# Kernel tuning notes

Measured on AMD Instinct MI355X. Metric: run time of the kernel, lower is better.

The kernel has to match this reference:

```python
import jax, jax.numpy as jnp
import numpy as np

DIM = 384
NUM_HEADS = 12
HEAD_DIM = 32
MID = NUM_HEADS * HEAD_DIM
RES = (32, 32)


def _relative_position_index(res):
    Hh, Ww = res
    coords = np.stack(np.meshgrid(np.arange(Hh), np.arange(Ww), indexing='ij'))  # 2,H,W
    cf = coords.reshape(2, -1)
    rel = cf[:, :, None] - cf[:, None, :]  # 2,N,N
    rel = rel.transpose(1, 2, 0).astype(np.int64)
    rel[:, :, 0] += Hh - 1
    rel[:, :, 1] += Ww - 1
    rel[:, :, 0] *= 2 * Ww - 1
    return rel.sum(-1)  # N,N


def setup_inputs() -> dict:
    key = jax.random.key(0)
    ks = jax.random.split(key, 8)
    B = 8
    Hh, Ww = RES
    table_size = (2 * Hh - 1) * (2 * Ww - 1)
    x = jax.random.normal(ks[0], (B, DIM, Hh, Ww), dtype=jnp.float32)
    wq = jax.random.normal(ks[1], (MID, DIM), dtype=jnp.float32) * 0.02
    bq = jnp.zeros((MID,), dtype=jnp.float32)
    wkv = jax.random.normal(ks[2], (2 * MID, DIM), dtype=jnp.float32) * 0.02
    bkv = jnp.zeros((2 * MID,), dtype=jnp.float32)
    wproj = jax.random.normal(ks[3], (DIM, MID), dtype=jnp.float32) * 0.02
    bproj = jnp.zeros((DIM,), dtype=jnp.float32)
    bias_table = jax.random.normal(ks[4], (table_size, NUM_HEADS), dtype=jnp.float32) * 0.02
    rel_index = jnp.asarray(_relative_position_index(RES), dtype=jnp.int32)  # N,N
    return {"x": x, "wq": wq, "bq": bq, "wkv": wkv, "bkv": bkv,
            "wproj": wproj, "bproj": bproj, "bias_table": bias_table,
            "rel_index": rel_index}


def reference(x, wq, bq, wkv, bkv, wproj, bproj, bias_table, rel_index):
    B, C, Hh, Ww = x.shape
    N = Hh * Ww
    scale = HEAD_DIM ** -0.5
    xf = x.reshape(B, C, N)  # B,C,N
    # 1x1 convs == channelwise linear
    q = jnp.einsum('oc,bcn->bon', wq, xf) + bq[None, :, None]          # B,MID,N
    kv = jnp.einsum('oc,bcn->bon', wkv, xf) + bkv[None, :, None]       # B,2*MID,N
    q = q.reshape(B, NUM_HEADS, HEAD_DIM, N).transpose(0, 1, 3, 2)     # B,h,N,d
    kv = kv.reshape(B, 2, NUM_HEADS, HEAD_DIM, N)
    k = kv[:, 0].transpose(0, 1, 3, 2)                                  # B,h,N,d
    v = kv[:, 1].transpose(0, 1, 3, 2)                                  # B,h,N,d
    attn = jnp.einsum('bhnd,bhmd->bhnm', q, k) * scale                  # B,h,N,N
    rel_bias = bias_table[rel_index.reshape(-1)].reshape(N, N, NUM_HEADS)
    attn = attn + rel_bias.transpose(2, 0, 1)[None]                     # + h,N,N bias
    attn = jax.nn.softmax(attn, axis=-1)
    out = jnp.einsum('bhnm,bhmd->bhnd', attn, v)                        # B,h,N,d
    out = out.transpose(0, 1, 3, 2).reshape(B, MID, N)                  # B,MID,N
    out = jnp.einsum('om,bmn->bon', wproj, out) + bproj[None, :, None]  # B,DIM,N
    return out.reshape(B, C, Hh, Ww)
```

## Files before the change

kernel.cpp:

```cpp
#include <hip/hip_runtime.h>

typedef __bf16 bf16;
typedef __bf16 bf16x8 __attribute__((ext_vector_type(8)));
typedef __bf16 bf16x4 __attribute__((ext_vector_type(4)));
typedef float  f32x4  __attribute__((ext_vector_type(4)));

static constexpr int NB = 8;
static constexpr int NH = 12;
static constexpr int HD = 32;
static constexpr int NN = 1024;
static constexpr int NC = 384;
static constexpr int NTBL = 3969;

static constexpr float LOG2E = 1.4426950408889634f;
static constexpr float QSC   = (float)(0.17677669529663687 * 1.4426950408889634);

static constexpr size_t XT_N   = (size_t)NB*NN*NC;
static constexpr size_t WQKV_N = (size_t)3*NC*NC;
static constexpr size_t WP_N   = (size_t)NC*NC;
static constexpr size_t QKV_N  = (size_t)NB*NH*NN*HD;

static constexpr size_t XT_OFF   = 0;
static constexpr size_t WQKV_OFF = XT_OFF + XT_N;
static constexpr size_t WP_OFF   = WQKV_OFF + WQKV_N;
static constexpr size_t Q_OFF    = WP_OFF + WP_N;
static constexpr size_t K_OFF    = Q_OFF + QKV_N;
static constexpr size_t V_OFF    = K_OFF + QKV_N;
static constexpr size_t AO_OFF   = V_OFF + QKV_N;

#define MFMA16(a,b,c) __builtin_amdgcn_mfma_f32_16x16x32_bf16(a,b,c,0,0,0)

static __device__ inline float fast_exp2(float x) {
#if __has_builtin(__builtin_amdgcn_exp2f)
    return __builtin_amdgcn_exp2f(x);
#else
    return exp2f(x);
#endif
}

__global__ __launch_bounds__(256) void cast_all_kernel(const float* __restrict__ x,
                                                       const float* __restrict__ wq,
                                                       const float* __restrict__ wkv,
                                                       const float* __restrict__ wproj,
                                                       bf16* __restrict__ xt,
                                                       bf16* __restrict__ wqkv,
                                                       bf16* __restrict__ wp)
{
    __shared__ bf16 T[64][68];
    const int t = threadIdx.x;
    if (blockIdx.x >= 768) {
        const size_t i = ((size_t)(blockIdx.x - 768) * 256 + t) * 4;
        if (i >= WQKV_N + WP_N) return;
        const float* src; bf16* dst;
        if (i < (size_t)NC*NC)      { src = wq + i;                     dst = wqkv + i; }
        else if (i < WQKV_N)        { src = wkv + (i - (size_t)NC*NC);  dst = wqkv + i; }
        else                        { src = wproj + (i - WQKV_N);       dst = wp + (i - WQKV_N); }
        float4 v = *(const float4*)src;
        bf16x4 o; o[0] = (bf16)v.x; o[1] = (bf16)v.y; o[2] = (bf16)v.z; o[3] = (bf16)v.w;
        *(bf16x4*)dst = o;
        return;
    }
    const int bid = blockIdx.x;
    const int b = bid / 96, rem = bid % 96, ct = rem >> 4, nt = rem & 15;
    const int c0 = ct * 64, n0 = nt * 64;
    const float* Xb = x + (size_t)b * NC * NN;
    const int nl = t & 63, c4 = (t >> 6) * 4;
#pragma unroll
    for (int i = 0; i < 4; ++i) {
        const int c = c4 + i * 16;
        bf16x4 v;
#pragma unroll
        for (int j = 0; j < 4; ++j)
            v[j] = (bf16)Xb[(size_t)(c0 + c + j) * NN + n0 + nl];
        *(bf16x4*)&T[nl][c] = v;
    }
    __syncthreads();
    const int n = t >> 2;
#pragma unroll
    for (int i = 0; i < 2; ++i) {
        const int cg = (t & 3) * 8 + i * 32;
        bf16x4 a = *(const bf16x4*)&T[n][cg];
        bf16x4 bv = *(const bf16x4*)&T[n][cg + 4];
        bf16x8 vv = __builtin_shufflevector(a, bv, 0, 1, 2, 3, 4, 5, 6, 7);
        *(bf16x8*)&xt[((size_t)b * NN + n0 + n) * NC + c0 + cg] = vv;
    }
}

__global__ __launch_bounds__(256) void qkv_gemm_kernel(
    const bf16* __restrict__ W, const bf16* __restrict__ Xt,
    const float* __restrict__ bq, const float* __restrict__ bkv,
    bf16* __restrict__ Qd, bf16* __restrict__ Kd, bf16* __restrict__ Vd)
{
    __shared__ bf16 As[64][40];
    __shared__ bf16 Bs[128][40];
    const int t = threadIdx.x;
    const int w = t >> 6, lane = t & 63, g = lane >> 4, l16 = lane & 15;
    const int wm = w >> 1, wn = w & 1;
    const int n0g = blockIdx.x * 128;
    const int b = n0g >> 10, n0 = n0g & 1023;
    const int o0 = blockIdx.y * 64;
    const bf16* Xb = Xt + (size_t)b * NN * NC;

    const int ar = t >> 2, ac = (t & 3) * 8;

    f32x4 acc[2][4] = {};

    bf16x8 aw = *(const bf16x8*)&W[(size_t)(o0 + ar) * NC + ac];
    bf16x8 bw[2];
#pragma unroll
    for (int i = 0; i < 2; ++i) {
        const int s = t + i * 256, r = s >> 2, cc = (s & 3) * 8;
        bw[i] = *(const bf16x8*)&Xb[(size_t)(n0 + r) * NC + cc];
    }

    for (int k0 = 0; k0 < NC; k0 += 32) {
        __syncthreads();
        *(bf16x8*)&As[ar][ac] = aw;
#pragma unroll
        for (int i = 0; i < 2; ++i) {
            const int s = t + i * 256, r = s >> 2, cc = (s & 3) * 8;
            *(bf16x8*)&Bs[r][cc] = bw[i];
        }
        __syncthreads();
        if (k0 + 32 < NC) {
            aw = *(const bf16x8*)&W[(size_t)(o0 + ar) * NC + k0 + 32 + ac];
#pragma unroll
            for (int i = 0; i < 2; ++i) {
                const int s = t + i * 256, r = s >> 2, cc = (s & 3) * 8;
                bw[i] = *(const bf16x8*)&Xb[(size_t)(n0 + r) * NC + k0 + 32 + cc];
            }
        }
        bf16x8 a0 = *(const bf16x8*)&As[wm*32      + l16][g*8];
        bf16x8 a1 = *(const bf16x8*)&As[wm*32 + 16 + l16][g*8];
#pragma unroll
        for (int sn = 0; sn < 4; ++sn) {
            bf16x8 bf = *(const bf16x8*)&Bs[wn*64 + sn*16 + l16][g*8];
            acc[0][sn] = MFMA16(a0, bf, acc[0][sn]);
            acc[1][sn] = MFMA16(a1, bf, acc[1][sn]);
        }
    }

#pragma unroll
    for (int sm = 0; sm < 2; ++sm)
#pragma unroll
    for (int sn = 0; sn < 4; ++sn) {
        const int col   = n0 + wn*64 + sn*16 + l16;
        const int obase = o0 + wm*32 + sm*16 + g*4;
        f32x4 v = acc[sm][sn];
        if (obase < 384) {
            const int hh = obase >> 5, d = obase & 31;
            bf16x4 o4;
#pragma unroll
            for (int r = 0; r < 4; ++r) o4[r] = (bf16)((v[r] + bq[obase + r]) * QSC);
            *(bf16x4*)&Qd[(((size_t)b*NH + hh)*NN + col)*HD + d] = o4;
        } else if (obase < 768) {
            const int oo = obase - 384; const int hh = oo >> 5, d = oo & 31;
            bf16x4 o4;
#pragma unroll
            for (int r = 0; r < 4; ++r) o4[r] = (bf16)(v[r] + bkv[oo + r]);
            *(bf16x4*)&Kd[(((size_t)b*NH + hh)*NN + col)*HD + d] = o4;
        } else {
            const int oo = obase - 768; const int hh = oo >> 5, d = oo & 31;
#pragma unroll
            for (int r = 0; r < 4; ++r)
                Vd[(((size_t)b*NH + hh)*HD + d + r)*NN + col] = (bf16)(v[r] + bkv[obase - 384 + r]);
        }
    }
}

__global__ __launch_bounds__(512, 8) void attn_kernel(
    const bf16* __restrict__ Qg, const bf16* __restrict__ Kg, const bf16* __restrict__ Vg,
    const float* __restrict__ bias_table, bf16* __restrict__ AOt)
{
    __shared__ unsigned int pairTu[63][63];
    __shared__ bf16 Ks[128][40];
    __shared__ bf16 Vs[2][32][72];

    const int t = threadIdx.x;
    const int w = t >> 6, lane = t & 63, g = lane >> 4, l16 = lane & 15;

    const int bid = blockIdx.x;
    const int nid = (bid & 7) * 96 + (bid >> 3);
    const int qt = nid & 7;
    const int hb = nid >> 3;
    const int h = hb % 12, b = hb / 12;

    const bf16* Qb = Qg + ((size_t)(b*NH + h)) * NN * HD;
    const bf16* Kb = Kg + ((size_t)(b*NH + h)) * NN * HD;
    const bf16* Vb = Vg + ((size_t)(b*NH + h)) * HD * NN;

    const int kr = t >> 2, kc2 = (t & 3) * 8;
    const int vd = t >> 4, vmi = (t & 15) * 8;
    const int vsub = vmi >> 6, vmm = vmi & 63;
    const int vqa = ((vmm >> 5) & 1) * 32 + ((vmm >> 2) & 3) * 8 + ((vmm >> 4) & 1) * 4;

    bf16x8 sregK = *(const bf16x8*)&Kb[(size_t)kr * HD + kc2];
    bf16x8 sregV = *(const bf16x8*)&Vb[(size_t)vd * NN + vmi];

    const int q0 = qt * 128;
    const int n_s = q0 + w*16 + l16;
    const bf16x8 qfrag = *(const bf16x8*)&Qb[(size_t)n_s * HD + g*8];

    for (int idx = t; idx < 63 * 62; idx += 512) {
        const int dj = idx / 62, dip = idx % 62;
        bf16 lo = (bf16)(bias_table[(size_t)((dip + 1) * 63 + dj) * NH + h] * LOG2E);
        bf16 hi = (bf16)(bias_table[(size_t)(dip * 63 + dj) * NH + h] * LOG2E);
        pairTu[dj][dip] = (unsigned)__builtin_bit_cast(unsigned short, lo)
                        | ((unsigned)__builtin_bit_cast(unsigned short, hi) << 16);
    }

    const int i1w = (q0 >> 5) + (w >> 1);
    const int j1 = ((w & 1) << 4) | l16;
    const int jA63 = (j1 + 31 - 4*g) * 63;

    bf16x8 vones;
#pragma unroll
    for (int e = 0; e < 8; ++e) vones[e] = (bf16)1.0f;

    f32x4 oacc[2] = {};
    f32x4 oacc_l = {};

    for (int ph = 0; ph < 8; ++ph) {
        __syncthreads();
        *(bf16x8*)&Ks[kr][kc2] = sregK;
        { bf16x4 vlo = __builtin_shufflevector(sregV, sregV, 0, 1, 2, 3);
          bf16x4 vhi = __builtin_shufflevector(sregV, sregV, 4, 5, 6, 7);
          *(bf16x4*)&Vs[vsub][vd][vqa]     = vlo;
          *(bf16x4*)&Vs[vsub][vd][vqa + 8] = vhi; }
        __syncthreads();
        if (ph < 7) {
            const int m1 = (ph + 1) * 128;
            sregK = *(const bf16x8*)&Kb[(size_t)(m1 + kr) * HD + kc2];
            sregV = *(const bf16x8*)&Vb[(size_t)vd * NN + m1 + vmi];
        }

#pragma unroll
        for (int sub = 0; sub < 2; ++sub) {
            const int it = 2 * ph + sub;
            const bf16 (*Vsp)[72] = Vs[sub];
            const int dip = i1w - 2*it + 30;
            const unsigned* pAp = &pairTu[0][0] + jA63 + dip;

            f32x4 bacc[4];
#pragma unroll
            for (int r = 0; r < 4; ++r) {
                const unsigned prA = pAp[-63 * r];
                const unsigned prB = pAp[-63 * r - 1008];
                bacc[0][r] = __uint_as_float(prA << 16);
                bacc[2][r] = __uint_as_float(prA & 0xFFFF0000u);
                bacc[1][r] = __uint_as_float(prB << 16);
                bacc[3][r] = __uint_as_float(prB & 0xFFFF0000u);
            }

            float p[4][4];
#pragma unroll
            for (int sc = 0; sc < 4; ++sc) {
                bf16x8 kf = *(const bf16x8*)&Ks[sub*64 + sc*16 + l16][g*8];
                f32x4 z = MFMA16(kf, qfrag, bacc[sc]);
#pragma unroll
                for (int r = 0; r < 4; ++r) p[sc][r] = fast_exp2(z[r]);
            }

#pragma unroll
            for (int kc = 0; kc < 2; ++kc) {
                bf16x8 pa;
#pragma unroll
                for (int r = 0; r < 4; ++r) {
                    pa[r]     = (bf16)p[2*kc][r];
                    pa[4 + r] = (bf16)p[2*kc + 1][r];
                }
#pragma unroll
                for (int ds = 0; ds < 2; ++ds) {
                    bf16x8 vf = *(const bf16x8*)&Vsp[ds*16 + l16][kc*32 + 8*g];
                    oacc[ds] = MFMA16(pa, vf, oacc[ds]);
                }
                oacc_l = MFMA16(pa, vones, oacc_l);
            }
        }
    }

    float rin[4];
#pragma unroll
    for (int r = 0; r < 4; ++r) rin[r] = 1.0f / oacc_l[r];

    const int nrow = q0 + w*16 + g*4;
#pragma unroll
    for (int ds = 0; ds < 2; ++ds) {
        const int c = h*HD + ds*16 + l16;
#pragma unroll
        for (int r = 0; r < 4; ++r)
            AOt[((size_t)b*NN + nrow + r) * NC + c] = (bf16)(oacc[ds][r] * rin[r]);
    }
}

__global__ __launch_bounds__(256) void proj_gemm_kernel(
    const bf16* __restrict__ W, const bf16* __restrict__ AOt,
    const float* __restrict__ bproj, float* __restrict__ out)
{
    __shared__ bf16 As[64][40];
    __shared__ bf16 Bs[128][40];
    const int t = threadIdx.x;
    const int w = t >> 6, lane = t & 63, g = lane >> 4, l16 = lane & 15;
    const int wm = w >> 1, wn = w & 1;
    const int n0g = blockIdx.x * 128;
    const int b = n0g >> 10, n0 = n0g & 1023;
    const int o0 = blockIdx.y * 64;
    const bf16* Ab = AOt + (size_t)b * NN * NC;

    const int ar = t >> 2, ac = (t & 3) * 8;

    f32x4 acc[2][4] = {};

    bf16x8 aw = *(const bf16x8*)&W[(size_t)(o0 + ar) * NC + ac];
    bf16x8 bw[2];
#pragma unroll
    for (int i = 0; i < 2; ++i) {
        const int s = t + i * 256, r = s >> 2, cc = (s & 3) * 8;
        bw[i] = *(const bf16x8*)&Ab[(size_t)(n0 + r) * NC + cc];
    }

    for (int k0 = 0; k0 < NC; k0 += 32) {
        __syncthreads();
        *(bf16x8*)&As[ar][ac] = aw;
#pragma unroll
        for (int i = 0; i < 2; ++i) {
            const int s = t + i * 256, r = s >> 2, cc = (s & 3) * 8;
            *(bf16x8*)&Bs[r][cc] = bw[i];
        }
        __syncthreads();
        if (k0 + 32 < NC) {
            aw = *(const bf16x8*)&W[(size_t)(o0 + ar) * NC + k0 + 32 + ac];
#pragma unroll
            for (int i = 0; i < 2; ++i) {
                const int s = t + i * 256, r = s >> 2, cc = (s & 3) * 8;
                bw[i] = *(const bf16x8*)&Ab[(size_t)(n0 + r) * NC + k0 + 32 + cc];
            }
        }
        bf16x8 a0 = *(const bf16x8*)&As[wm*32      + l16][g*8];
        bf16x8 a1 = *(const bf16x8*)&As[wm*32 + 16 + l16][g*8];
#pragma unroll
        for (int sn = 0; sn < 4; ++sn) {
            bf16x8 bf = *(const bf16x8*)&Bs[wn*64 + sn*16 + l16][g*8];
            acc[0][sn] = MFMA16(a0, bf, acc[0][sn]);
            acc[1][sn] = MFMA16(a1, bf, acc[1][sn]);
        }
    }

#pragma unroll
    for (int sm = 0; sm < 2; ++sm)
#pragma unroll
    for (int sn = 0; sn < 4; ++sn) {
        const int col   = n0 + wn*64 + sn*16 + l16;
        const int obase = o0 + wm*32 + sm*16 + g*4;
        f32x4 v = acc[sm][sn];
#pragma unroll
        for (int r = 0; r < 4; ++r)
            out[((size_t)b*NC + obase + r)*NN + col] = v[r] + bproj[obase + r];
    }
}

extern "C" void kernel_launch(void* const* d_in, const int* in_sizes, int n_in,
                              void* d_out, int out_size, void* d_ws, size_t ws_size,
                              hipStream_t stream)
{
    const float* x          = (const float*)d_in[0];
    const float* wq         = (const float*)d_in[1];
    const float* bq         = (const float*)d_in[2];
    const float* wkv        = (const float*)d_in[3];
    const float* bkv        = (const float*)d_in[4];
    const float* wproj      = (const float*)d_in[5];
    const float* bproj      = (const float*)d_in[6];
    const float* bias_table = (const float*)d_in[7];
    float* out = (float*)d_out;

    bf16* wsb  = (bf16*)d_ws;
    bf16* Xt   = wsb + XT_OFF;
    bf16* Wqkv = wsb + WQKV_OFF;
    bf16* Wp   = wsb + WP_OFF;
    bf16* Qd   = wsb + Q_OFF;
    bf16* Kd   = wsb + K_OFF;
    bf16* Vd   = wsb + V_OFF;
    bf16* AOt  = wsb + AO_OFF;

    cast_all_kernel<<<dim3(768 + 576), 256, 0, stream>>>(x, wq, wkv, wproj, Xt, Wqkv, Wp);
    qkv_gemm_kernel<<<dim3(64, 18), 256, 0, stream>>>(Wqkv, Xt, bq, bkv, Qd, Kd, Vd);
    attn_kernel<<<dim3(768), 512, 0, stream>>>(Qd, Kd, Vd, bias_table, AOt);
    proj_gemm_kernel<<<dim3(64, 6), 256, 0, stream>>>(Wp, AOt, bproj, out);
}
```

Baseline: 67.40 us.

## Use direct global-to-LDS loads with swizzle and 128x128 tiles in GEMMs

```diff
diff --git a/kernel.cpp b/kernel.cpp
--- a/kernel.cpp
+++ b/kernel.cpp
@@ -36,6 +36,12 @@
 #else
     return exp2f(x);
 #endif
+}
+
+static __device__ __forceinline__ void gload16(const bf16* g, bf16* l) {
+    __builtin_amdgcn_global_load_lds(
+        (const __attribute__((address_space(1))) void*)g,
+        (__attribute__((address_space(3))) void*)l, 16, 0, 0);
 }
 
 __global__ __launch_bounds__(256) void cast_all_kernel(const float* __restrict__ x,
@@ -91,61 +97,50 @@
     const float* __restrict__ bq, const float* __restrict__ bkv,
     bf16* __restrict__ Qd, bf16* __restrict__ Kd, bf16* __restrict__ Vd)
 {
-    __shared__ bf16 As[64][40];
-    __shared__ bf16 Bs[128][40];
+    __shared__ bf16 As[128 * 32];
+    __shared__ bf16 Bs[128 * 32];
     const int t = threadIdx.x;
     const int w = t >> 6, lane = t & 63, g = lane >> 4, l16 = lane & 15;
     const int wm = w >> 1, wn = w & 1;
     const int n0g = blockIdx.x * 128;
     const int b = n0g >> 10, n0 = n0g & 1023;
-    const int o0 = blockIdx.y * 64;
+    const int o0 = blockIdx.y * 128;
     const bf16* Xb = Xt + (size_t)b * NN * NC;
 
-    const int ar = t >> 2, ac = (t & 3) * 8;
-
-    f32x4 acc[2][4] = {};
-
-    bf16x8 aw = *(const bf16x8*)&W[(size_t)(o0 + ar) * NC + ac];
-    bf16x8 bw[2];
-#pragma unroll
-    for (int i = 0; i < 2; ++i) {
-        const int s = t + i * 256, r = s >> 2, cc = (s & 3) * 8;
-        bw[i] = *(const bf16x8*)&Xb[(size_t)(n0 + r) * NC + cc];
-    }
+    const int srow = lane >> 2;
+    const int scol = (((lane & 3) ^ ((lane >> 3) & 3))) * 8;
+    const int rsel = (g ^ ((l16 >> 1) & 3)) * 8;
+
+    f32x4 acc[4][4] = {};
 
     for (int k0 = 0; k0 < NC; k0 += 32) {
-        __syncthreads();
-        *(bf16x8*)&As[ar][ac] = aw;
-#pragma unroll
-        for (int i = 0; i < 2; ++i) {
-            const int s = t + i * 256, r = s >> 2, cc = (s & 3) * 8;
-            *(bf16x8*)&Bs[r][cc] = bw[i];
-        }
-        __syncthreads();
-        if (k0 + 32 < NC) {
-            aw = *(const bf16x8*)&W[(size_t)(o0 + ar) * NC + k0 + 32 + ac];
-#pragma unroll
-            for (int i = 0; i < 2; ++i) {
-                const int s = t + i * 256, r = s >> 2, cc = (s & 3) * 8;
-                bw[i] = *(const bf16x8*)&Xb[(size_t)(n0 + r) * NC + k0 + 32 + cc];
-            }
-        }
-        bf16x8 a0 = *(const bf16x8*)&As[wm*32      + l16][g*8];
-        bf16x8 a1 = *(const bf16x8*)&As[wm*32 + 16 + l16][g*8];
-#pragma unroll
-        for (int sn = 0; sn < 4; ++sn) {
-            bf16x8 bf = *(const bf16x8*)&Bs[wn*64 + sn*16 + l16][g*8];
-            acc[0][sn] = MFMA16(a0, bf, acc[0][sn]);
-            acc[1][sn] = MFMA16(a1, bf, acc[1][sn]);
-        }
-    }
-
-#pragma unroll
-    for (int sm = 0; sm < 2; ++sm)
+#pragma unroll
+        for (int j = 0; j < 2; ++j) {
+            const int ra = 32 * w + 16 * j;
+            gload16(&W [(size_t)(o0 + ra + srow) * NC + k0 + scol], &As[ra * 32]);
+            gload16(&Xb[(size_t)(n0 + ra + srow) * NC + k0 + scol], &Bs[ra * 32]);
+        }
+        __syncthreads();
+        bf16x8 a[4], bb[4];
+#pragma unroll
+        for (int s = 0; s < 4; ++s) {
+            a[s]  = *(const bf16x8*)&As[(wm*64 + s*16 + l16) * 32 + rsel];
+            bb[s] = *(const bf16x8*)&Bs[(wn*64 + s*16 + l16) * 32 + rsel];
+        }
+#pragma unroll
+        for (int sm = 0; sm < 4; ++sm)
+#pragma unroll
+            for (int sn = 0; sn < 4; ++sn)
+                acc[sm][sn] = MFMA16(a[sm], bb[sn], acc[sm][sn]);
+        __syncthreads();
+    }
+
+#pragma unroll
+    for (int sm = 0; sm < 4; ++sm)
 #pragma unroll
     for (int sn = 0; sn < 4; ++sn) {
         const int col   = n0 + wn*64 + sn*16 + l16;
-        const int obase = o0 + wm*32 + sm*16 + g*4;
+        const int obase = o0 + wm*64 + sm*16 + g*4;
         f32x4 v = acc[sm][sn];
         if (obase < 384) {
             const int hh = obase >> 5, d = obase & 31;
@@ -252,6 +247,7 @@
                 bacc[3][r] = __uint_as_float(prB & 0xFFFF0000u);
             }
 
+            __builtin_amdgcn_s_setprio(1);
             float p[4][4];
 #pragma unroll
             for (int sc = 0; sc < 4; ++sc) {
@@ -276,6 +272,7 @@
                 }
                 oacc_l = MFMA16(pa, vones, oacc_l);
             }
+            __builtin_amdgcn_s_setprio(0);
         }
     }
 
@@ -297,61 +294,50 @@
     const bf16* __restrict__ W, const bf16* __restrict__ AOt,
     const float* __restrict__ bproj, float* __restrict__ out)
 {
-    __shared__ bf16 As[64][40];
-    __shared__ bf16 Bs[128][40];
+    __shared__ bf16 As[128 * 32];
+    __shared__ bf16 Bs[128 * 32];
     const int t = threadIdx.x;
     const int w = t >> 6, lane = t & 63, g = lane >> 4, l16 = lane & 15;
     const int wm = w >> 1, wn = w & 1;
     const int n0g = blockIdx.x * 128;
     const int b = n0g >> 10, n0 = n0g & 1023;
-    const int o0 = blockIdx.y * 64;
+    const int o0 = blockIdx.y * 128;
     const bf16* Ab = AOt + (size_t)b * NN * NC;
 
-    const int ar = t >> 2, ac = (t & 3) * 8;
-
-    f32x4 acc[2][4] = {};
-
-    bf16x8 aw = *(const bf16x8*)&W[(size_t)(o0 + ar) * NC + ac];
-    bf16x8 bw[2];
-#pragma unroll
-    for (int i = 0; i < 2; ++i) {
-        const int s = t + i * 256, r = s >> 2, cc = (s & 3) * 8;
-        bw[i] = *(const bf16x8*)&Ab[(size_t)(n0 + r) * NC + cc];
-    }
+    const int srow = lane >> 2;
+    const int scol = (((lane & 3) ^ ((lane >> 3) & 3))) * 8;
+    const int rsel = (g ^ ((l16 >> 1) & 3)) * 8;
+
+    f32x4 acc[4][4] = {};
 
     for (int k0 = 0; k0 < NC; k0 += 32) {
-        __syncthreads();
-        *(bf16x8*)&As[ar][ac] = aw;
-#pragma unroll
-        for (int i = 0; i < 2; ++i) {
-            const int s = t + i * 256, r = s >> 2, cc = (s & 3) * 8;
-            *(bf16x8*)&Bs[r][cc] = bw[i];
-        }
-        __syncthreads();
-        if (k0 + 32 < NC) {
-            aw = *(const bf16x8*)&W[(size_t)(o0 + ar) * NC + k0 + 32 + ac];
-#pragma unroll
-            for (int i = 0; i < 2; ++i) {
-                const int s = t + i * 256, r = s >> 2, cc = (s & 3) * 8;
-                bw[i] = *(const bf16x8*)&Ab[(size_t)(n0 + r) * NC + k0 + 32 + cc];
-            }
-        }
-        bf16x8 a0 = *(const bf16x8*)&As[wm*32      + l16][g*8];
-        bf16x8 a1 = *(const bf16x8*)&As[wm*32 + 16 + l16][g*8];
-#pragma unroll
-        for (int sn = 0; sn < 4; ++sn) {
-            bf16x8 bf = *(const bf16x8*)&Bs[wn*64 + sn*16 + l16][g*8];
-            acc[0][sn] = MFMA16(a0, bf, acc[0][sn]);
-            acc[1][sn] = MFMA16(a1, bf, acc[1][sn]);
-        }
-    }
-
-#pragma unroll
-    for (int sm = 0; sm < 2; ++sm)
+#pragma unroll
+        for (int j = 0; j < 2; ++j) {
+            const int ra = 32 * w + 16 * j;
+            gload16(&W [(size_t)(o0 + ra + srow) * NC + k0 + scol], &As[ra * 32]);
+            gload16(&Ab[(size_t)(n0 + ra + srow) * NC + k0 + scol], &Bs[ra * 32]);
+        }
+        __syncthreads();
+        bf16x8 a[4], bb[4];
+#pragma unroll
+        for (int s = 0; s < 4; ++s) {
+            a[s]  = *(const bf16x8*)&As[(wm*64 + s*16 + l16) * 32 + rsel];
+            bb[s] = *(const bf16x8*)&Bs[(wn*64 + s*16 + l16) * 32 + rsel];
+        }
+#pragma unroll
+        for (int sm = 0; sm < 4; ++sm)
+#pragma unroll
+            for (int sn = 0; sn < 4; ++sn)
+                acc[sm][sn] = MFMA16(a[sm], bb[sn], acc[sm][sn]);
+        __syncthreads();
+    }
+
+#pragma unroll
+    for (int sm = 0; sm < 4; ++sm)
 #pragma unroll
     for (int sn = 0; sn < 4; ++sn) {
         const int col   = n0 + wn*64 + sn*16 + l16;
-        const int obase = o0 + wm*32 + sm*16 + g*4;
+        const int obase = o0 + wm*64 + sm*16 + g*4;
         f32x4 v = acc[sm][sn];
 #pragma unroll
         for (int r = 0; r < 4; ++r)
@@ -383,7 +369,7 @@
     bf16* AOt  = wsb + AO_OFF;
 
     cast_all_kernel<<<dim3(768 + 576), 256, 0, stream>>>(x, wq, wkv, wproj, Xt, Wqkv, Wp);
-    qkv_gemm_kernel<<<dim3(64, 18), 256, 0, stream>>>(Wqkv, Xt, bq, bkv, Qd, Kd, Vd);
+    qkv_gemm_kernel<<<dim3(64, 9), 256, 0, stream>>>(Wqkv, Xt, bq, bkv, Qd, Kd, Vd);
     attn_kernel<<<dim3(768), 512, 0, stream>>>(Qd, Kd, Vd, bias_table, AOt);
-    proj_gemm_kernel<<<dim3(64, 6), 256, 0, stream>>>(Wp, AOt, bproj, out);
-}
+    proj_gemm_kernel<<<dim3(64, 3), 256, 0, stream>>>(Wp, AOt, bproj, out);
+}
```

Result: slower. 74.71 us (+10.8%).
